# Kernel optimization log

Hardware: AMD Instinct MI355X
Metric: run time of the kernel (lower is better)

Reference implementation:

```python
import jax, jax.numpy as jnp
import numpy as np

WINDOW = (6, 7, 7)  # (agent_size, window_size, window_size)
HEADS = 8           # dim // dim_head = 256 // 32


def _relative_position_index(ws):
    d, h, w = ws
    coords = np.stack(np.meshgrid(np.arange(d), np.arange(h), np.arange(w), indexing='ij'))
    cf = coords.reshape(3, -1)                      # [3, n]
    rel = cf[:, :, None] - cf[:, None, :]           # [3, n, n]
    rel = rel.transpose(1, 2, 0).copy()             # [n, n, 3]
    rel[..., 0] += d - 1
    rel[..., 1] += h - 1
    rel[..., 2] += w - 1
    rel[..., 0] *= (2 * h - 1) * (2 * w - 1)
    rel[..., 1] *= (2 * w - 1)
    return rel.sum(-1)                              # [n, n] int

REL_IDX = jnp.asarray(_relative_position_index(WINDOW))


def setup_inputs() -> dict:
    key = jax.random.key(0)
    ks = jax.random.split(key, 7)
    dim = 256
    n_bias = (2 * WINDOW[0] - 1) * (2 * WINDOW[1] - 1) * (2 * WINDOW[2] - 1)  # 1859
    s = 0.02
    return {
        'x': jax.random.normal(ks[0], (2, 6, 12, 12, 7, 7, dim), jnp.float32),
        'Wq': jax.random.normal(ks[1], (dim, dim), jnp.float32) * s,
        'bq': jax.random.normal(ks[2], (dim,), jnp.float32) * s,
        'Wkv': jax.random.normal(ks[3], (dim, 2 * dim), jnp.float32) * s,
        'bkv': jax.random.normal(ks[4], (2 * dim,), jnp.float32) * s,
        'Wout': jax.random.normal(ks[5], (dim, dim), jnp.float32) * s,
        'bias_table': jax.random.normal(ks[6], (n_bias, HEADS), jnp.float32) * s,
    }


def reference(x, Wq, bq, Wkv, bkv, Wout, bias_table):
    b, l, gx, gy, w1, w2, d = x.shape
    h = HEADS
    dh = d // h
    n = l * w1 * w2
    B = b * gx * gy
    # 'b l x y w1 w2 d -> (b x y) (l w1 w2) d'  (agent-major token order)
    xt = jnp.transpose(x, (0, 2, 3, 1, 4, 5, 6)).reshape(B, n, d)
    q = xt @ Wq + bq                                  # [B, n, d]
    kv = xt @ Wkv + bkv                               # [B, n, 2d]
    k, v = kv[..., :d], kv[..., d:]
    split = lambda t: t.reshape(B, n, h, dh).transpose(0, 2, 1, 3)  # [B, h, n, dh]
    q, k, v = split(q), split(k), split(v)
    scale = dh ** -0.5
    sim = jnp.einsum('bhid,bhjd->bhij', q * scale, k)  # [B, h, n, n]
    bias = bias_table[REL_IDX]                         # [n, n, h]
    sim = sim + jnp.transpose(bias, (2, 0, 1))[None]
    attn = jax.nn.softmax(sim, axis=-1)
    out = jnp.einsum('bhij,bhjd->bhid', attn, v)       # [B, h, n, dh]
    out = out.transpose(0, 2, 1, 3).reshape(B, n, d) @ Wout
    # '(b x y) (l w1 w2) d -> b l x y w1 w2 d'
    out = out.reshape(b, gx, gy, l, w1, w2, d)
    return jnp.transpose(out, (0, 3, 1, 2, 4, 5, 6))
```

## Files before the change

### kernel.cpp

```cpp
#include <hip/hip_runtime.h>
#include <hip/hip_bf16.h>

#define DIM    256
#define NWIN   294
#define BWIN   288
#define MROWS  (BWIN * NWIN)
#define MPAD   84736
#define NHEADS 8
#define DH     32
#define NBIAS  1859
#define QPAD   304
#define KPAD   304
#define KPITCH (KPAD * DH)

typedef __attribute__((ext_vector_type(8))) short  short8;
typedef __attribute__((ext_vector_type(4))) float  f32x4;

__device__ __forceinline__ unsigned short f2bf(float f) {
    unsigned int u = __float_as_uint(f);
    u += 0x7FFFu + ((u >> 16) & 1u);
    return (unsigned short)(u >> 16);
}

__device__ __forceinline__ unsigned pk2bf(float a, float b) {
    __hip_bfloat162 h = __float22bfloat162_rn(float2{a, b});
    unsigned u;
    __builtin_memcpy(&u, &h, 4);
    return u;
}

__device__ __forceinline__ void gl_lds16(const void* g, void* l) {
    __builtin_amdgcn_global_load_lds((const __attribute__((address_space(1))) unsigned int*)g,
                                     (__attribute__((address_space(3))) unsigned int*)l,
                                     16, 0, 0);
}

__device__ __forceinline__ int xcd_swizzle(int orig, int nwg) {
    const int xcd = orig & 7, idx = orig >> 3;
    const int q = nwg >> 3, r = nwg & 7;
    return (xcd < r) ? (xcd * (q + 1) + idx) : (r * (q + 1) + (xcd - r) * q + idx);
}

__device__ __forceinline__ void stage_tile(const unsigned short* aBase, const unsigned short* bBase,
                                           unsigned short* As_, unsigned short* Bs_, int w, int k0)
{
#pragma unroll
    for (int i = 0; i < 4; ++i) {
        const int c = w * 4 + i;
        gl_lds16(aBase + (size_t)c * 8 * 256 + k0, As_ + c * 512);
        gl_lds16(bBase + (size_t)c * 8 * 256 + k0, Bs_ + c * 512);
    }
}

__device__ __forceinline__ void tile_mfma(const unsigned short* As_, const unsigned short* Bs_,
                                          int wm, int wn, int quad, int l15, f32x4 (&acc)[4][4])
{
#pragma unroll
    for (int c2 = 0; c2 < 2; ++c2) {
        const int kk = c2 * 32 + quad * 8;
        short8 a[4], b[4];
#pragma unroll
        for (int mi = 0; mi < 4; ++mi)
            a[mi] = *(const short8*)&As_[(wm * 64 + mi * 16 + l15) * 64 + kk];
#pragma unroll
        for (int ni = 0; ni < 4; ++ni)
            b[ni] = *(const short8*)&Bs_[(wn * 64 + ni * 16 + l15) * 64 + kk];
#pragma unroll
        for (int mi = 0; mi < 4; ++mi)
#pragma unroll
            for (int ni = 0; ni < 4; ++ni)
                acc[mi][ni] = __builtin_amdgcn_mfma_f32_16x16x32_bf16(a[mi], b[ni], acc[mi][ni], 0, 0, 0);
    }
}

__global__ __launch_bounds__(256) void prep_x(const float* __restrict__ x,
                                              unsigned short* __restrict__ Xb)
{
    const int g   = blockIdx.x * 256 + threadIdx.x;
    const int row = g >> 5;
    const int col = (g & 31) * 8;
    if (row >= MPAD) return;
    uint4 pk;
    if (row < MROWS) {
        const int bw = row / NWIN, rw = row - bw * NWIN;
        const int bb = bw / 144,  r2 = bw - bb * 144;
        const int gxi = r2 / 12,  gyi = r2 - gxi * 12;
        const int lz = rw / 49,   r3 = rw - lz * 49;
        const int wa = r3 / 7,    wb = r3 - wa * 7;
        const float* src = x + ((((((size_t)bb * 6 + lz) * 12 + gxi) * 12 + gyi) * 7 + wa) * 7 + wb) * DIM + col;
        const float4 f0 = *(const float4*)(src);
        const float4 f1 = *(const float4*)(src + 4);
        pk.x = pk2bf(f0.x, f0.y);
        pk.y = pk2bf(f0.z, f0.w);
        pk.z = pk2bf(f1.x, f1.y);
        pk.w = pk2bf(f1.z, f1.w);
    } else {
        pk = (uint4){0u, 0u, 0u, 0u};
    }
    *(uint4*)(Xb + (size_t)row * 256 + col) = pk;
}

__global__ __launch_bounds__(256) void prep_w(const float* __restrict__ Wq,
                                              const float* __restrict__ Wkv,
                                              const float* __restrict__ Wout,
                                              unsigned short* __restrict__ Wt,
                                              unsigned short* __restrict__ Wot)
{
    const int g = blockIdx.x * 256 + threadIdx.x;
    if (g < 768 * 256) {
        const int n = g >> 8, k = g & 255;
        const float v = (n < 256) ? Wq[k * 256 + n] : Wkv[k * 512 + (n - 256)];
        Wt[g] = f2bf(v);
    } else {
        const int g2 = g - 768 * 256;
        const int n = g2 >> 8, k = g2 & 255;
        Wot[g2] = f2bf(Wout[k * 256 + n]);
    }
}

__global__ __launch_bounds__(256) void prep_bias(const float* __restrict__ bias_table,
                                                 float* __restrict__ biasT)
{
    const int g = blockIdx.x * 256 + threadIdx.x;
    if (g >= NHEADS * QPAD * QPAD) return;
    const int k = g % QPAD;
    const int q = (g / QPAD) % QPAD;
    const int h = g / (QPAD * QPAD);
    float v = 0.f;
    if (q < NWIN && k < NWIN) {
        const int ql = q / 49, qr = q - ql * 49, qa = qr / 7, qb = qr - qa * 7;
        const int kl = k / 49, kr = k - kl * 49, ka = kr / 7, kb = kr - ka * 7;
        const int idx = 169 * (ql - kl + 5) + 13 * (qa - ka + 6) + (qb - kb + 6);
        v = bias_table[idx * NHEADS + h] * 1.44269504088896f;
    }
    biasT[g] = v;
}

__global__ __launch_bounds__(256) void prep_zero(unsigned short* __restrict__ Kb)
{
    const int g = blockIdx.x * 256 + threadIdx.x;
    if (g >= BWIN * NHEADS * 40) return;
    const int bh = g / 40, r = g - bh * 40;
    *(uint4*)(Kb + (size_t)bh * KPITCH + NWIN * DH + r * 8) = (uint4){0u, 0u, 0u, 0u};
}

__global__ __launch_bounds__(256) void gemm_qkv(
    const unsigned short* __restrict__ Xb, const unsigned short* __restrict__ Wt,
    const float* __restrict__ bq, const float* __restrict__ bkv,
    unsigned short* __restrict__ Qb, unsigned short* __restrict__ Kb,
    unsigned short* __restrict__ Vtb)
{
    __shared__ __align__(16) unsigned short As[2][128 * 64];
    __shared__ __align__(16) unsigned short Bs[2][128 * 64];

    const int wg = xcd_swizzle(blockIdx.x, 662 * 6);
    const int bn = wg % 6;
    const int bm = wg / 6;
    const int tileM = bm * 128;
    const int tileN = bn * 128;

    const int t    = threadIdx.x;
    const int w    = t >> 6;
    const int lane = t & 63;
    const int quad = lane >> 4;
    const int l15  = lane & 15;
    const int wm   = w >> 1, wn = w & 1;

    const int rA = lane >> 3;
    const int kA = (lane & 7) * 8;
    const unsigned short* aBase = Xb + ((size_t)tileM + rA) * 256 + kA;
    const unsigned short* bBase = Wt + ((size_t)tileN + rA) * 256 + kA;

    f32x4 acc[4][4] = {};

    stage_tile(aBase, bBase, As[0], Bs[0], w, 0);
    __syncthreads();
#pragma unroll
    for (int kb = 0; kb < 3; ++kb) {
        const int cur = kb & 1;
        stage_tile(aBase, bBase, As[cur ^ 1], Bs[cur ^ 1], w, (kb + 1) * 64);
        tile_mfma(As[cur], Bs[cur], wm, wn, quad, l15, acc);
        __syncthreads();
    }
    tile_mfma(As[1], Bs[1], wm, wn, quad, l15, acc);

    const int colB = tileN + wn * 64;
    float bias[4];
#pragma unroll
    for (int ni = 0; ni < 4; ++ni) {
        const int n = colB + ni * 16 + l15;
        bias[ni] = (n < 256) ? bq[n] : bkv[n - 256];
    }
    const int rowB = tileM + wm * 64 + quad * 4;
#pragma unroll
    for (int mi = 0; mi < 4; ++mi) {
        const int row0 = rowB + mi * 16;
        if (row0 < MROWS) {
            const int bw0 = row0 / NWIN;
            const int rw0 = row0 - bw0 * NWIN;
            const bool same = (rw0 <= NWIN - 4);
#pragma unroll
            for (int ni = 0; ni < 4; ++ni) {
                const int n = colB + ni * 16 + l15;
                const int ch = n & 255;
                const int hd = ch >> 5, di = ch & 31;
                if (n < 256) {
                    if (same) {
                        unsigned short* p = Qb + ((size_t)(bw0 * NHEADS + hd) * NWIN + rw0) * DH + di;
#pragma unroll
                        for (int r = 0; r < 4; ++r)
                            p[r * DH] = f2bf(acc[mi][ni][r] + bias[ni]);
                    } else {
#pragma unroll
                        for (int r = 0; r < 4; ++r) {
                            const int row = row0 + r;
                            if (row < MROWS) {
                                const int bw = row / NWIN, rw = row - bw * NWIN;
                                Qb[((size_t)(bw * NHEADS + hd) * NWIN + rw) * DH + di] =
                                    f2bf(acc[mi][ni][r] + bias[ni]);
                            }
                        }
                    }
                } else if (n < 512) {
                    if (same) {
                        unsigned short* p = Kb + ((size_t)(bw0 * NHEADS + hd) * KPAD + rw0) * DH + di;
#pragma unroll
                        for (int r = 0; r < 4; ++r)
                            p[r * DH] = f2bf(acc[mi][ni][r] + bias[ni]);
                    } else {
#pragma unroll
                        for (int r = 0; r < 4; ++r) {
                            const int row = row0 + r;
                            if (row < MROWS) {
                                const int bw = row / NWIN, rw = row - bw * NWIN;
                                Kb[((size_t)(bw * NHEADS + hd) * KPAD + rw) * DH + di] =
                                    f2bf(acc[mi][ni][r] + bias[ni]);
                            }
                        }
                    }
                } else {
                    if (same) {
                        unsigned short* p = Vtb + ((size_t)(bw0 * NHEADS + hd) * DH + di) * NWIN + rw0;
                        const unsigned lo = pk2bf(acc[mi][ni][0] + bias[ni], acc[mi][ni][1] + bias[ni]);
                        const unsigned hi = pk2bf(acc[mi][ni][2] + bias[ni], acc[mi][ni][3] + bias[ni]);
                        *(unsigned*)(p)     = lo;
                        *(unsigned*)(p + 2) = hi;
                    } else {
#pragma unroll
                        for (int r = 0; r < 4; ++r) {
                            const int row = row0 + r;
                            if (row < MROWS) {
                                const int bw = row / NWIN, rw = row - bw * NWIN;
                                Vtb[((size_t)(bw * NHEADS + hd) * DH + di) * NWIN + rw] =
                                    f2bf(acc[mi][ni][r] + bias[ni]);
                            }
                        }
                    }
                }
            }
        }
    }
}

__global__ __launch_bounds__(256) void attn_kernel(
    const unsigned short* __restrict__ Qb, const unsigned short* __restrict__ Kb,
    const unsigned short* __restrict__ Vtb, const float* __restrict__ biasT,
    unsigned short* __restrict__ Ob)
{
    const int bh   = blockIdx.x;
    const int bwin = bh >> 3;
    const int h    = bh & 7;

    __shared__ __align__(16) unsigned short Vts[32 * 328];

    const int t    = threadIdx.x;
    const int w    = t >> 6;
    const int lane = t & 63;
    const int quad = lane >> 4;
    const int l15  = lane & 15;

    {
        const unsigned short* Vg = Vtb + (size_t)bh * (DH * NWIN);
        for (int i = t; i < 32 * 80; i += 256) {
            const int d = i / 80, c = i - d * 80;
            const int kt = c >> 3, qd = (c >> 1) & 3, hf = c & 1;
            const int kb = kt * 32 + hf * 16 + qd * 4;
            unsigned int u0 = 0u, u1 = 0u;
            if (kb + 3 < NWIN) {
                u0 = *(const unsigned int*)(Vg + d * NWIN + kb);
                u1 = *(const unsigned int*)(Vg + d * NWIN + kb + 2);
            } else if (kb < NWIN) {
                unsigned short r0 = Vg[d * NWIN + kb];
                unsigned short r1 = (kb + 1 < NWIN) ? Vg[d * NWIN + kb + 1] : (unsigned short)0;
                unsigned short r2 = (kb + 2 < NWIN) ? Vg[d * NWIN + kb + 2] : (unsigned short)0;
                u0 = (unsigned int)r0 | ((unsigned int)r1 << 16);
                u1 = (unsigned int)r2;
            }
            unsigned int* dst = (unsigned int*)(Vts + d * 328 + c * 4);
            dst[0] = u0; dst[1] = u1;
        }
    }
    __syncthreads();

    const float SL2E = 0.25503486f;
    const unsigned short* Qg = Qb + (size_t)bh * (NWIN * DH);
    const unsigned short* Kg = Kb + (size_t)bh * KPITCH;
    const float* biasH = biasT + (size_t)h * QPAD * QPAD;
    const short8 ones = (short8){0x3F80,0x3F80,0x3F80,0x3F80,0x3F80,0x3F80,0x3F80,0x3F80};

#pragma unroll
    for (int r5 = 0; r5 < 5; ++r5) {
        const int it = 4 * r5 + w;
        if (it < 19) {
            short8 qf;
            const int qrow = it * 16 + l15;
            if (qrow < NWIN) qf = *(const short8*)(Qg + qrow * DH + quad * 8);
            else             qf = (short8){0,0,0,0,0,0,0,0};

            const float* bb = biasH + (size_t)qrow * QPAD;

            f32x4 S[19];
#pragma unroll
            for (int jt = 0; jt < 19; ++jt) {
                const short8 kf = *(const short8*)(Kg + (jt * 16 + l15) * DH + quad * 8);
                S[jt] = __builtin_amdgcn_mfma_f32_16x16x32_bf16(kf, qf, (f32x4){0.f,0.f,0.f,0.f}, 0, 0, 0);
            }

            unsigned pk0[20], pk1[20];
            pk0[19] = 0u; pk1[19] = 0u;
#pragma unroll
            for (int jt = 0; jt < 19; ++jt) {
                const f32x4 b4 = *(const f32x4*)(bb + jt * 16 + quad * 4);
                float p0 = exp2f(fmaf(S[jt][0], SL2E, b4[0]));
                float p1 = exp2f(fmaf(S[jt][1], SL2E, b4[1]));
                float p2 = exp2f(fmaf(S[jt][2], SL2E, b4[2]));
                float p3 = exp2f(fmaf(S[jt][3], SL2E, b4[3]));
                if (jt == 18) {
                    if (quad * 4 + 0 >= 6) p0 = 0.f;
                    if (quad * 4 + 1 >= 6) p1 = 0.f;
                    if (quad * 4 + 2 >= 6) p2 = 0.f;
                    if (quad * 4 + 3 >= 6) p3 = 0.f;
                }
                pk0[jt] = pk2bf(p0, p1);
                pk1[jt] = pk2bf(p2, p3);
            }

            f32x4 o0 = {0.f,0.f,0.f,0.f}, o1 = {0.f,0.f,0.f,0.f}, o2 = {0.f,0.f,0.f,0.f};
#pragma unroll
            for (int kt = 0; kt < 10; ++kt) {
                uint4 pw;
                pw.x = pk0[2 * kt];
                pw.y = pk1[2 * kt];
                pw.z = pk0[2 * kt + 1];
                pw.w = pk1[2 * kt + 1];
                short8 pa;
                __builtin_memcpy(&pa, &pw, 16);
                const short8 v0 = *(const short8*)(Vts + l15 * 328 + kt * 32 + quad * 8);
                const short8 v1 = *(const short8*)(Vts + (16 + l15) * 328 + kt * 32 + quad * 8);
                o0 = __builtin_amdgcn_mfma_f32_16x16x32_bf16(pa, v0, o0, 0, 0, 0);
                o1 = __builtin_amdgcn_mfma_f32_16x16x32_bf16(pa, v1, o1, 0, 0, 0);
                o2 = __builtin_amdgcn_mfma_f32_16x16x32_bf16(pa, ones, o2, 0, 0, 0);
            }

#pragma unroll
            for (int r = 0; r < 4; ++r) {
                const int rg = it * 16 + quad * 4 + r;
                if (rg < NWIN) {
                    const float inv = 1.0f / o2[r];
                    unsigned short* op = Ob + ((size_t)bwin * NWIN + rg) * DIM + h * DH;
                    op[l15]      = f2bf(o0[r] * inv);
                    op[16 + l15] = f2bf(o1[r] * inv);
                }
            }
        }
    }
}

__global__ __launch_bounds__(256) void gemm_out(
    const unsigned short* __restrict__ Ob, const unsigned short* __restrict__ Wot,
    float* __restrict__ out)
{
    __shared__ __align__(16) unsigned short As[2][128 * 64];
    __shared__ __align__(16) unsigned short Bs[2][128 * 64];

    const int wg = xcd_swizzle(blockIdx.x, 662 * 2);
    const int bn = wg & 1;
    const int bm = wg >> 1;
    const int tileM = bm * 128;
    const int tileN = bn * 128;

    const int t    = threadIdx.x;
    const int w    = t >> 6;
    const int lane = t & 63;
    const int quad = lane >> 4;
    const int l15  = lane & 15;
    const int wm   = w >> 1, wn = w & 1;

    const int rA = lane >> 3;
    const int kA = (lane & 7) * 8;
    const unsigned short* aBase = Ob  + ((size_t)tileM + rA) * 256 + kA;
    const unsigned short* bBase = Wot + ((size_t)tileN + rA) * 256 + kA;

    f32x4 acc[4][4] = {};

    stage_tile(aBase, bBase, As[0], Bs[0], w, 0);
    __syncthreads();
#pragma unroll
    for (int kb = 0; kb < 3; ++kb) {
        const int cur = kb & 1;
        stage_tile(aBase, bBase, As[cur ^ 1], Bs[cur ^ 1], w, (kb + 1) * 64);
        tile_mfma(As[cur], Bs[cur], wm, wn, quad, l15, acc);
        __syncthreads();
    }
    tile_mfma(As[1], Bs[1], wm, wn, quad, l15, acc);

    const int colB = tileN + wn * 64;
    const int rowB = tileM + wm * 64 + quad * 4;
#pragma unroll
    for (int mi = 0; mi < 4; ++mi) {
#pragma unroll
        for (int r = 0; r < 4; ++r) {
            const int row = rowB + mi * 16 + r;
            if (row < MROWS) {
                const int bw = row / NWIN, rw = row - bw * NWIN;
                const int bb = bw / 144,  r2 = bw - bb * 144;
                const int gxi = r2 / 12,  gyi = r2 - gxi * 12;
                const int lz = rw / 49,   r3 = rw - lz * 49;
                const int wa = r3 / 7,    wb = r3 - wa * 7;
                float* orow = out + ((((((size_t)bb * 6 + lz) * 12 + gxi) * 12 + gyi) * 7 + wa) * 7 + wb) * DIM;
#pragma unroll
                for (int ni = 0; ni < 4; ++ni)
                    orow[colB + ni * 16 + l15] = acc[mi][ni][r];
            }
        }
    }
}

extern "C" void kernel_launch(void* const* d_in, const int* in_sizes, int n_in,
                              void* d_out, int out_size, void* d_ws, size_t ws_size,
                              hipStream_t stream)
{
    const float* x          = (const float*)d_in[0];
    const float* Wq         = (const float*)d_in[1];
    const float* bq         = (const float*)d_in[2];
    const float* Wkv        = (const float*)d_in[3];
    const float* bkv        = (const float*)d_in[4];
    const float* Wout       = (const float*)d_in[5];
    const float* bias_table = (const float*)d_in[6];
    float* out = (float*)d_out;

    const size_t planePad = (size_t)MPAD * DIM;
    const size_t plane    = (size_t)MROWS * DIM;
    const size_t planeK   = (size_t)BWIN * NHEADS * KPITCH;
    unsigned short* Xb  = (unsigned short*)d_ws;
    unsigned short* Qb  = Xb + planePad;
    unsigned short* Kb  = Qb + plane;
    unsigned short* Vtb = Kb + planeK;
    unsigned short* Ob  = Vtb + plane;
    unsigned short* Wt  = Ob + planePad;
    unsigned short* Wot = Wt + 768 * 256;
    float*          biasT = (float*)(Wot + 256 * 256);

    prep_x<<<MPAD / 8, 256, 0, stream>>>(x, Xb);
    prep_w<<<1024, 256, 0, stream>>>(Wq, Wkv, Wout, Wt, Wot);
    prep_bias<<<(NHEADS * QPAD * QPAD + 255) / 256, 256, 0, stream>>>(bias_table, biasT);
    prep_zero<<<(BWIN * NHEADS * 40 + 255) / 256, 256, 0, stream>>>(Kb);
    gemm_qkv<<<662 * 6, 256, 0, stream>>>(Xb, Wt, bq, bkv, Qb, Kb, Vtb);
    attn_kernel<<<BWIN * NHEADS, 256, 0, stream>>>(Qb, Kb, Vtb, biasT, Ob);
    gemm_out<<<662 * 2, 256, 0, stream>>>(Ob, Wot, out);
}
```

Baseline: 421.2 us.

## Stage K in LDS, fragment-order V layout, and software-pipeline QK^T with bias prefetch

The attention kernel now copies each head's K tile into shared memory in MFMA fragment order using the gl_lds16 helper, and stores V^T in a lane-contiguous fragment layout so each lane reads one contiguous 16-byte chunk. The score loop is software-pipelined: the MFMA for the next key tile is issued while exp2 runs on the current one, and bias rows are prefetched five tiles ahead in a rotating register buffer. This replaces 19 live S accumulators with two, lowering register pressure, and cuts repeated global K reads from each of the four waves. It adds LDS use (about 39 KB) and relies on gl_lds16 issuing async copies that are covered by the existing __syncthreads, which could limit blocks per CU.

```diff
diff --git a/kernel.cpp b/kernel.cpp
--- a/kernel.cpp
+++ b/kernel.cpp
@@ -271,7 +271,8 @@
     const int bwin = bh >> 3;
     const int h    = bh & 7;
 
-    __shared__ __align__(16) unsigned short Vts[32 * 328];
+    __shared__ __align__(16) unsigned short KsF[19 * 512];
+    __shared__ __align__(16) unsigned short VtsF[10 * 1024];
 
     const int t    = threadIdx.x;
     const int w    = t >> 6;
@@ -279,6 +280,12 @@
     const int quad = lane >> 4;
     const int l15  = lane & 15;
 
+    {
+        const unsigned short* Kg = Kb + (size_t)bh * KPITCH;
+        const unsigned short* src0 = Kg + (size_t)l15 * DH + quad * 8;
+        for (int jt = w; jt < 19; jt += 4)
+            gl_lds16(src0 + jt * 16 * DH, &KsF[jt * 512]);
+    }
     {
         const unsigned short* Vg = Vtb + (size_t)bh * (DH * NWIN);
         for (int i = t; i < 32 * 80; i += 256) {
@@ -296,7 +303,8 @@
                 u0 = (unsigned int)r0 | ((unsigned int)r1 << 16);
                 u1 = (unsigned int)r2;
             }
-            unsigned int* dst = (unsigned int*)(Vts + d * 328 + c * 4);
+            unsigned int* dst = (unsigned int*)(VtsF + kt * 1024 + (d >> 4) * 512
+                                                + (qd * 16 + (d & 15)) * 8 + hf * 4);
             dst[0] = u0; dst[1] = u1;
         }
     }
@@ -304,9 +312,10 @@
 
     const float SL2E = 0.25503486f;
     const unsigned short* Qg = Qb + (size_t)bh * (NWIN * DH);
-    const unsigned short* Kg = Kb + (size_t)bh * KPITCH;
     const float* biasH = biasT + (size_t)h * QPAD * QPAD;
     const short8 ones = (short8){0x3F80,0x3F80,0x3F80,0x3F80,0x3F80,0x3F80,0x3F80,0x3F80};
+    const unsigned short* ksLane = KsF + lane * 8;
+    const unsigned short* vtLane = VtsF + lane * 8;
 
 #pragma unroll
     for (int r5 = 0; r5 < 5; ++r5) {
@@ -317,24 +326,34 @@
             if (qrow < NWIN) qf = *(const short8*)(Qg + qrow * DH + quad * 8);
             else             qf = (short8){0,0,0,0,0,0,0,0};
 
-            const float* bb = biasH + (size_t)qrow * QPAD;
-
-            f32x4 S[19];
-#pragma unroll
-            for (int jt = 0; jt < 19; ++jt) {
-                const short8 kf = *(const short8*)(Kg + (jt * 16 + l15) * DH + quad * 8);
-                S[jt] = __builtin_amdgcn_mfma_f32_16x16x32_bf16(kf, qf, (f32x4){0.f,0.f,0.f,0.f}, 0, 0, 0);
-            }
+            const float* bb = biasH + (size_t)qrow * QPAD + quad * 4;
 
             unsigned pk0[20], pk1[20];
             pk0[19] = 0u; pk1[19] = 0u;
+
+            f32x4 bpre[5];
+#pragma unroll
+            for (int p = 0; p < 5; ++p)
+                bpre[p] = *(const f32x4*)(bb + p * 16);
+
+            short8 kf0 = *(const short8*)(ksLane);
+            f32x4 Scur = __builtin_amdgcn_mfma_f32_16x16x32_bf16(kf0, qf, (f32x4){0.f,0.f,0.f,0.f}, 0, 0, 0);
+
 #pragma unroll
             for (int jt = 0; jt < 19; ++jt) {
-                const f32x4 b4 = *(const f32x4*)(bb + jt * 16 + quad * 4);
-                float p0 = exp2f(fmaf(S[jt][0], SL2E, b4[0]));
-                float p1 = exp2f(fmaf(S[jt][1], SL2E, b4[1]));
-                float p2 = exp2f(fmaf(S[jt][2], SL2E, b4[2]));
-                float p3 = exp2f(fmaf(S[jt][3], SL2E, b4[3]));
+                f32x4 Snext = Scur;
+                if (jt < 18) {
+                    const short8 kfn = *(const short8*)(ksLane + (jt + 1) * 512);
+                    Snext = __builtin_amdgcn_mfma_f32_16x16x32_bf16(kfn, qf, (f32x4){0.f,0.f,0.f,0.f}, 0, 0, 0);
+                }
+                const f32x4 b4 = bpre[jt % 5];
+                if (jt + 5 < 19)
+                    bpre[jt % 5] = *(const f32x4*)(bb + (jt + 5) * 16);
+
+                float p0 = exp2f(fmaf(Scur[0], SL2E, b4[0]));
+                float p1 = exp2f(fmaf(Scur[1], SL2E, b4[1]));
+                float p2 = exp2f(fmaf(Scur[2], SL2E, b4[2]));
+                float p3 = exp2f(fmaf(Scur[3], SL2E, b4[3]));
                 if (jt == 18) {
                     if (quad * 4 + 0 >= 6) p0 = 0.f;
                     if (quad * 4 + 1 >= 6) p1 = 0.f;
@@ -343,6 +362,7 @@
                 }
                 pk0[jt] = pk2bf(p0, p1);
                 pk1[jt] = pk2bf(p2, p3);
+                Scur = Snext;
             }
 
             f32x4 o0 = {0.f,0.f,0.f,0.f}, o1 = {0.f,0.f,0.f,0.f}, o2 = {0.f,0.f,0.f,0.f};
@@ -355,8 +375,8 @@
                 pw.w = pk1[2 * kt + 1];
                 short8 pa;
                 __builtin_memcpy(&pa, &pw, 16);
-                const short8 v0 = *(const short8*)(Vts + l15 * 328 + kt * 32 + quad * 8);
-                const short8 v1 = *(const short8*)(Vts + (16 + l15) * 328 + kt * 32 + quad * 8);
+                const short8 v0 = *(const short8*)(vtLane + kt * 1024);
+                const short8 v1 = *(const short8*)(vtLane + kt * 1024 + 512);
                 o0 = __builtin_amdgcn_mfma_f32_16x16x32_bf16(pa, v0, o0, 0, 0, 0);
                 o1 = __builtin_amdgcn_mfma_f32_16x16x32_bf16(pa, v1, o1, 0, 0, 0);
                 o2 = __builtin_amdgcn_mfma_f32_16x16x32_bf16(pa, ones, o2, 0, 0, 0);
```

New measurement: 416.8 us. About the same (-1.0%).
